# Kernel tuning notes

Hardware: AMD Instinct MI355X
Metric: run time of the kernel (lower is better)

Reference implementation:

```python
import jax, jax.numpy as jnp
import numpy as np

B, T, S = 4, 128, 8192
HID, NH, NKV, HD = 2560, 8, 4, 256
INTER = 10240
WINDOW = 1024
SOFTCAP = 50.0
SCALING = 256 ** -0.5  # query_pre_attn_scalar ** -0.5
EPS = 1e-6
NEG = -2.3819763e38  # large negative for masking (matches Gemma mask value)
ROPE_THETA = 10000.0


def _rmsnorm(x, w):
    xf = x.astype(jnp.float32)
    o = xf * jax.lax.rsqrt(jnp.mean(xf * xf, axis=-1, keepdims=True) + EPS)
    return (o * (1.0 + w.astype(jnp.float32))).astype(x.dtype)


def _rope(x, cos, sin):
    # split-half rotation, matching torch apply_rotary_emb (chunk->complex->mul)
    d2 = x.shape[-1] // 2
    x1, x2 = x[..., :d2], x[..., d2:]
    c = cos[None, :, None, :]  # [1,T,1,D/2]
    s = sin[None, :, None, :]
    return jnp.concatenate([x1 * c - x2 * s, x1 * s + x2 * c], axis=-1)


def setup_inputs() -> dict:
    key = jax.random.key(0)
    ks = jax.random.split(key, 14)
    hidden_states = jax.random.normal(ks[0], (B, T, HID), jnp.float32)
    kv_write_indices = jnp.arange(T, dtype=jnp.int32)
    k_cache = jnp.zeros((B, S, NKV, HD), jnp.float32)
    v_cache = jnp.zeros((B, S, NKV, HD), jnp.float32)
    # rotary tables for positions 0..T-1
    inv = 1.0 / (ROPE_THETA ** (np.arange(0, HD, 2)[: HD // 2].astype(np.float32) / HD))
    fr = np.outer(np.arange(T, dtype=np.float32), inv).astype(np.float32)
    freqs_cos = jnp.asarray(np.cos(fr))
    freqs_sin = jnp.asarray(np.sin(fr))
    # masks: query i sits at absolute position i; cache slots >= T are unwritten
    qpos = jnp.arange(T)[:, None]
    kpos = jnp.arange(S)[None, :]
    causal = kpos <= qpos
    local = causal & ((qpos - kpos) < WINDOW)
    mask = jnp.broadcast_to(jnp.where(causal, 0.0, NEG)[None, None], (B, 1, T, S)).astype(jnp.float32)
    local_mask = jnp.broadcast_to(jnp.where(local, 0.0, NEG)[None, None], (B, 1, T, S)).astype(jnp.float32)
    sc = 0.02
    w_qkv = sc * jax.random.normal(ks[1], ((NH + 2 * NKV) * HD, HID), jnp.float32)
    w_o = sc * jax.random.normal(ks[2], (HID, NH * HD), jnp.float32)
    q_norm_w = 0.1 * jax.random.normal(ks[3], (HD,), jnp.float32)
    k_norm_w = 0.1 * jax.random.normal(ks[4], (HD,), jnp.float32)
    in_ln_w = 0.1 * jax.random.normal(ks[5], (HID,), jnp.float32)
    post_attn_ln_w = 0.1 * jax.random.normal(ks[6], (HID,), jnp.float32)
    pre_ffw_ln_w = 0.1 * jax.random.normal(ks[7], (HID,), jnp.float32)
    post_ffw_ln_w = 0.1 * jax.random.normal(ks[8], (HID,), jnp.float32)
    w_gate = sc * jax.random.normal(ks[9], (INTER, HID), jnp.float32)
    w_up = sc * jax.random.normal(ks[10], (INTER, HID), jnp.float32)
    w_down = sc * jax.random.normal(ks[11], (HID, INTER), jnp.float32)
    return {
        "hidden_states": hidden_states, "freqs_cos": freqs_cos, "freqs_sin": freqs_sin,
        "kv_write_indices": kv_write_indices, "k_cache": k_cache, "v_cache": v_cache,
        "mask": mask, "local_mask": local_mask,
        "w_qkv": w_qkv, "w_o": w_o, "q_norm_w": q_norm_w, "k_norm_w": k_norm_w,
        "in_ln_w": in_ln_w, "post_attn_ln_w": post_attn_ln_w,
        "pre_ffw_ln_w": pre_ffw_ln_w, "post_ffw_ln_w": post_ffw_ln_w,
        "w_gate": w_gate, "w_up": w_up, "w_down": w_down,
    }


def reference(hidden_states, freqs_cos, freqs_sin, kv_write_indices, k_cache, v_cache,
              mask, local_mask, w_qkv, w_o, q_norm_w, k_norm_w, in_ln_w,
              post_attn_ln_w, pre_ffw_ln_w, post_ffw_ln_w, w_gate, w_up, w_down):
    b, t, _ = hidden_states.shape
    residual = hidden_states
    h = _rmsnorm(hidden_states, in_ln_w)
    qkv = h @ w_qkv.T
    q_sz, kv_sz = NH * HD, NKV * HD
    xq = qkv[..., :q_sz].reshape(b, t, NH, HD)
    xk = qkv[..., q_sz:q_sz + kv_sz].reshape(b, t, NKV, HD)
    xv = qkv[..., q_sz + kv_sz:].reshape(b, t, NKV, HD)
    xq = _rmsnorm(xq, q_norm_w)  # QK-norm
    xk = _rmsnorm(xk, k_norm_w)
    xq = _rope(xq, freqs_cos, freqs_sin)
    xk = _rope(xk, freqs_cos, freqs_sin)
    kc = k_cache.at[:, kv_write_indices].set(xk)  # index_copy_ on dim 1
    vc = v_cache.at[:, kv_write_indices].set(xv)
    g = NH // NKV
    q = (xq * SCALING).reshape(b, t, NKV, g, HD)
    # GQA without repeat_interleave: group dim g shares each kv head
    scores = jnp.einsum('btkgd,bskd->bkgts', q, kc)
    scores = SOFTCAP * jnp.tanh(scores / SOFTCAP)  # logit softcapping
    scores = scores + local_mask[:, :, None]  # LOCAL_SLIDING -> use local mask
    probs = jax.nn.softmax(scores.astype(jnp.float32), axis=-1).astype(q.dtype)
    attn = jnp.einsum('bkgts,bskd->btkgd', probs, vc).reshape(b, t, NH * HD)
    attn = attn @ w_o.T
    h = residual + _rmsnorm(attn, post_attn_ln_w)
    residual = h
    x = _rmsnorm(h, pre_ffw_ln_w)
    gate = jax.nn.gelu(x @ w_gate.T, approximate=True)
    mlp = (gate * (x @ w_up.T)) @ w_down.T
    return residual + _rmsnorm(mlp, post_ffw_ln_w)
```

## Files before the change

kernel.cpp:

```cpp
#include <hip/hip_runtime.h>
#include <hip/hip_bf16.h>

#define B_ 4
#define T_ 128
#define HID 2560
#define NH 8
#define NKV 4
#define HD 256
#define INTER 10240
#define MROWS 512
#define EPS 1e-6f

typedef float f32x4 __attribute__((ext_vector_type(4)));
typedef __bf16 bf16x8 __attribute__((ext_vector_type(8)));

__device__ __forceinline__ unsigned short f2bf(float f){
  unsigned int u = __builtin_bit_cast(unsigned int, f);
  u += 0x7fffu + ((u >> 16) & 1u);
  return (unsigned short)(u >> 16);
}
__device__ __forceinline__ float bf2f(unsigned short u){
  unsigned int x = ((unsigned int)u) << 16;
  return __builtin_bit_cast(float, x);
}
__device__ __forceinline__ unsigned int cvtpk(float lo, float hi){
  unsigned int r;
  asm("v_cvt_pk_bf16_f32 %0, %1, %2" : "=v"(r) : "v"(lo), "v"(hi));
  return r;
}
__device__ __forceinline__ void glds16(const void* g, void* l){
  __builtin_amdgcn_global_load_lds(
      (const __attribute__((address_space(1))) void*)g,
      (__attribute__((address_space(3))) void*)l, 16, 0, 0);
}

__device__ __forceinline__ float bsum256(float v, float* buf){
  #pragma unroll
  for (int o = 32; o; o >>= 1) v += __shfl_xor(v, o);
  __syncthreads();
  if ((threadIdx.x & 63) == 0) buf[threadIdx.x >> 6] = v;
  __syncthreads();
  return buf[0] + buf[1] + buf[2] + buf[3];
}


__global__ __launch_bounds__(256) void rms_in(
    const float* __restrict__ x, const float* __restrict__ w,
    unsigned short* __restrict__ out)
{
  __shared__ float buf[4];
  const int r = blockIdx.x, tid = threadIdx.x;
  const float* xp = x + (size_t)r * HID;
  float v[10]; float ss = 0.f;
  #pragma unroll
  for (int j = 0; j < 10; j++){ v[j] = xp[tid + j*256]; ss += v[j]*v[j]; }
  ss = bsum256(ss, buf);
  float s = rsqrtf(ss * (1.f/HID) + EPS);
  #pragma unroll
  for (int j = 0; j < 10; j++){
    int i = tid + j*256;
    out[((size_t)(i >> 5) * MROWS + r) * 32 + (i & 31)] = f2bf(v[j] * s * (1.f + w[i]));
  }
}

__global__ __launch_bounds__(256, 2) void gemm_big(
    const unsigned short* __restrict__ Ap,
    const float* __restrict__ B0,
    const float* __restrict__ B1,
    int n_hi,
    unsigned short* __restrict__ C,
    int N, int K, int klen)
{
  __shared__ char Bs4[4 * 16384];
  const int tid = threadIdx.x;
  const int bid = (blockIdx.x & 7) * ((int)gridDim.x >> 3) + (blockIdx.x >> 3);
  const int bm = (bid & 1) << 8;
  const int bn = (bid >> 1) << 7;
  const int kt0 = (blockIdx.y * klen) >> 5;
  const int nt = klen >> 5;

  const int w = tid >> 6, l = tid & 63;
  const float* Bb = (bn < n_hi) ? B0 : B1;
  const int bnr = (bn < n_hi) ? bn : (bn - n_hi);

  const int grow_l = l >> 3;
  const int gchunk = l & 7;

  const int wm = (w & 1) << 7;
  const int wn = (w >> 1) << 6;
  const int fr = l & 15, kq = l >> 4;

  const unsigned short* ApL = Ap + ((size_t)kt0 * MROWS + bm + wm + fr) * 32 + kq * 8;

  f32x4 acc[8][4];
  #pragma unroll
  for (int i = 0; i < 8; i++)
    #pragma unroll
    for (int j = 0; j < 4; j++)
      #pragma unroll
      for (int e = 0; e < 4; e++) acc[i][j][e] = 0.f;

  uint4 aR[8], aS[8];

#define ISSUE_A(dst, tt) { const unsigned short* ap = ApL + (size_t)(tt) * 16384; \
  dst[0] = *(const uint4*)(ap);        dst[1] = *(const uint4*)(ap + 512); \
  dst[2] = *(const uint4*)(ap + 1024); dst[3] = *(const uint4*)(ap + 1536); \
  dst[4] = *(const uint4*)(ap + 2048); dst[5] = *(const uint4*)(ap + 2560); \
  dst[6] = *(const uint4*)(ap + 3072); dst[7] = *(const uint4*)(ap + 3584); }
#define GLDS_B(tt, slot) { const int ktf = (kt0 + (tt)) << 5; \
  char* dstb = Bs4 + ((slot) << 14) + (w << 12); \
  _Pragma("unroll") for (int g = 0; g < 4; g++){ \
    int row = (w << 5) + (g << 3) + grow_l; \
    const float* src = Bb + (size_t)(bnr + row) * K + ktf + ((gchunk ^ (row & 7)) << 2); \
    glds16(src, dstb + (g << 10)); } }
#define VM(n) asm volatile("s_waitcnt vmcnt(" #n ")" ::: "memory")
#define COMPUTE(slot, aset) { const char* bb = Bs4 + ((slot) << 14); \
  bf16x8 bfv[4]; \
  _Pragma("unroll") for (int ni = 0; ni < 4; ni++){ \
    int row = wn + ni*16 + fr; \
    const char* rbase = bb + (row << 7); \
    int sw = row & 7; \
    f32x4 lo = *(const f32x4*)(rbase + ((( 2*kq   ) ^ sw) << 4)); \
    f32x4 hi = *(const f32x4*)(rbase + ((( 2*kq+1 ) ^ sw) << 4)); \
    union { unsigned int u[4]; bf16x8 v; } pk; \
    pk.u[0] = cvtpk(lo[0], lo[1]); pk.u[1] = cvtpk(lo[2], lo[3]); \
    pk.u[2] = cvtpk(hi[0], hi[1]); pk.u[3] = cvtpk(hi[2], hi[3]); \
    bfv[ni] = pk.v; } \
  __builtin_amdgcn_s_setprio(1); \
  _Pragma("unroll") for (int mi = 0; mi < 8; mi++){ \
    bf16x8 af = __builtin_bit_cast(bf16x8, aset[mi]); \
    _Pragma("unroll") for (int ni = 0; ni < 4; ni++) \
      acc[mi][ni] = __builtin_amdgcn_mfma_f32_16x16x32_bf16(af, bfv[ni], acc[mi][ni], 0, 0, 0); } \
  __builtin_amdgcn_s_setprio(0); }
#define MIN_(a,b) ((a)<(b)?(a):(b))

  ISSUE_A(aR, 0);
  GLDS_B(0, 0); GLDS_B(1, 1); GLDS_B(2, 2);
  ISSUE_A(aS, MIN_(1, nt-1));
  VM(16);
  __builtin_amdgcn_s_barrier();
  GLDS_B(MIN_(3, nt-1), 3);
  COMPUTE(0, aR);
  ISSUE_A(aR, MIN_(2, nt-1));
  VM(24);
  __builtin_amdgcn_s_barrier();
  GLDS_B(MIN_(4, nt-1), 0);
  COMPUTE(1, aS);
  for (int t = 2; t < nt; t += 2) {
    ISSUE_A(aS, MIN_(t+1, nt-1));
    VM(32);
    __builtin_amdgcn_s_barrier();
    GLDS_B(MIN_(t+3, nt-1), (t+3) & 3);
    COMPUTE(t & 3, aR);
    ISSUE_A(aR, MIN_(t+2, nt-1));
    VM(32);
    __builtin_amdgcn_s_barrier();
    GLDS_B(MIN_(t+4, nt-1), t & 3);
    COMPUTE((t+1) & 3, aS);
  }
#undef ISSUE_A
#undef GLDS_B
#undef VM
#undef COMPUTE
#undef MIN_

  unsigned short* Cp = C + (size_t)blockIdx.y * MROWS * N;
  #pragma unroll
  for (int mi = 0; mi < 8; mi++) {
    #pragma unroll
    for (int ni = 0; ni < 4; ni++) {
      int m = bm + wm + mi*16 + kq*4;
      int n = bn + wn + ni*16 + fr;
      #pragma unroll
      for (int i = 0; i < 4; i++)
        Cp[(size_t)(m + i) * N + n] = f2bf(acc[mi][ni][i]);
    }
  }
}

__global__ __launch_bounds__(64) void qkv_post(
    const unsigned short* __restrict__ qkvp,
    const float* __restrict__ fcos, const float* __restrict__ fsin,
    const float* __restrict__ qnw, const float* __restrict__ knw,
    float* __restrict__ qout, float* __restrict__ kT, float* __restrict__ vout)
{
  const int row = blockIdx.x;
  const int hh  = blockIdx.y;
  const int b = row >> 7, t = row & 127;
  const int l = threadIdx.x;
  const size_t MS = (size_t)MROWS * 4096;
  const unsigned short* src = qkvp + (size_t)row * 4096 + hh * 256;
  float x[4];
  #pragma unroll
  for (int j = 0; j < 4; j++){
    int d = l + j*64;
    float v = 0.f;
    #pragma unroll
    for (int s = 0; s < 8; s++) v += bf2f(src[d + s*MS]);
    x[j] = v;
  }
  if (hh >= 12) {
    float* vp = vout + ((size_t)(b*NKV + (hh-12)) * T_ + t) * HD;
    #pragma unroll
    for (int j = 0; j < 4; j++) vp[l + j*64] = x[j];
    return;
  }
  float ss = x[0]*x[0] + x[1]*x[1] + x[2]*x[2] + x[3]*x[3];
  #pragma unroll
  for (int o = 32; o; o >>= 1) ss += __shfl_xor(ss, o);
  float r = rsqrtf(ss * (1.f/HD) + EPS);
  const float* nw = (hh < 8) ? qnw : knw;
  #pragma unroll
  for (int j = 0; j < 4; j++){ int d = l + j*64; x[j] = x[j] * r * (1.f + nw[d]); }
  float c0 = fcos[t*128 + l],      s0 = fsin[t*128 + l];
  float c1 = fcos[t*128 + l + 64], s1 = fsin[t*128 + l + 64];
  float y0 = x[0]*c0 - x[2]*s0;
  float y2 = x[0]*s0 + x[2]*c0;
  float y1 = x[1]*c1 - x[3]*s1;
  float y3 = x[1]*s1 + x[3]*c1;
  if (hh < 8) {
    float* qp = qout + ((size_t)(b*NH + hh) * T_ + t) * HD;
    const float sc = 0.0625f;
    qp[l] = y0*sc; qp[l+64] = y1*sc; qp[l+128] = y2*sc; qp[l+192] = y3*sc;
  } else {
    float* kp = kT + (size_t)(b*NKV + (hh-8)) * HD * T_;
    kp[(size_t)(l)*T_ + t] = y0;  kp[(size_t)(l+64)*T_ + t] = y1;
    kp[(size_t)(l+128)*T_ + t] = y2; kp[(size_t)(l+192)*T_ + t] = y3;
  }
}

__global__ __launch_bounds__(128) void attn_fwd(
    const float* __restrict__ q, const float* __restrict__ kT,
    const float* __restrict__ V, unsigned short* __restrict__ att)
{
  const int id = blockIdx.x;
  const int t = id & 127;
  const int h = (id >> 7) & 7;
  const int b = id >> 10;
  const int kvh = h >> 1;
  const int tid = threadIdx.x;
  __shared__ float qs[256];
  __shared__ float sc[128];
  __shared__ float red[128];
  const float* qp = q + (size_t)id * HD;
  qs[tid] = qp[tid]; qs[tid + 128] = qp[tid + 128];
  __syncthreads();
  const float* kp = kT + (size_t)(b*NKV + kvh) * HD * T_;
  float dot = 0.f;
  const bool valid = (tid <= t);
  if (valid) {
    #pragma unroll 8
    for (int d = 0; d < 256; d++) dot += qs[d] * kp[(size_t)d*T_ + tid];
  }
  float score = valid ? 50.f * tanhf(dot * 0.02f) : -3.0e38f;
  sc[tid] = score; red[tid] = score;
  __syncthreads();
  for (int o = 64; o; o >>= 1){ if (tid < o) red[tid] = fmaxf(red[tid], red[tid+o]); __syncthreads(); }
  float m = red[0];
  __syncthreads();
  float p = valid ? __expf(score - m) : 0.f;
  sc[tid] = p; red[tid] = p;
  __syncthreads();
  for (int o = 64; o; o >>= 1){ if (tid < o) red[tid] += red[tid+o]; __syncthreads(); }
  float inv = 1.f / red[0];
  const float* vp = V + (size_t)(b*NKV + kvh) * T_ * HD;
  float a0 = 0.f, a1 = 0.f;
  for (int s = 0; s <= t; s++){
    float ps = sc[s];
    a0 += ps * vp[(size_t)s*HD + tid];
    a1 += ps * vp[(size_t)s*HD + tid + 128];
  }
  const int row = b*T_ + t;
  const int c0 = h*256 + tid, c1 = c0 + 128;
  att[((size_t)(c0 >> 5) * MROWS + row) * 32 + (c0 & 31)] = f2bf(a0 * inv);
  att[((size_t)(c1 >> 5) * MROWS + row) * 32 + (c1 & 31)] = f2bf(a1 * inv);
}

__global__ __launch_bounds__(256) void post_attn_k(
    const unsigned short* __restrict__ op, const float* __restrict__ hs,
    const float* __restrict__ wpost, const float* __restrict__ wpre,
    float* __restrict__ h2, unsigned short* __restrict__ xout)
{
  __shared__ float buf[4];
  const int r = blockIdx.x, tid = threadIdx.x;
  const size_t MS = (size_t)MROWS * HID;
  float o[10]; float ss = 0.f;
  #pragma unroll
  for (int j = 0; j < 10; j++){
    size_t i = (size_t)r*HID + tid + j*256;
    float v = 0.f;
    #pragma unroll
    for (int s = 0; s < 16; s++) v += bf2f(op[i + s*MS]);
    o[j] = v; ss += v*v;
  }
  ss = bsum256(ss, buf);
  float s = rsqrtf(ss*(1.f/HID) + EPS);
  float h[10]; float s2 = 0.f;
  #pragma unroll
  for (int j = 0; j < 10; j++){
    int i = tid + j*256;
    float hv = hs[(size_t)r*HID + i] + o[j]*s*(1.f + wpost[i]);
    h[j] = hv; h2[(size_t)r*HID + i] = hv; s2 += hv*hv;
  }
  s2 = bsum256(s2, buf);
  float sc2 = rsqrtf(s2*(1.f/HID) + EPS);
  #pragma unroll
  for (int j = 0; j < 10; j++){
    int i = tid + j*256;
    xout[((size_t)(i >> 5) * MROWS + r) * 32 + (i & 31)] = f2bf(h[j]*sc2*(1.f + wpre[i]));
  }
}

__global__ __launch_bounds__(256) void act_fuse(
    const unsigned short* __restrict__ gu,
    unsigned short* __restrict__ act)
{
  const int r = blockIdx.x;
  const int c0 = blockIdx.y * 2560;
  const size_t MS = (size_t)MROWS * 20480;
  const unsigned short* rowp = gu + (size_t)r * 20480;
  for (int c = c0 + threadIdx.x; c < c0 + 2560; c += 256){
    float g = 0.f, u = 0.f;
    #pragma unroll
    for (int s = 0; s < 4; s++){
      g += bf2f(rowp[s*MS + c]);
      u += bf2f(rowp[s*MS + c + INTER]);
    }
    float tt = tanhf(0.7978845608f * (g + 0.044715f * g*g*g));
    float ge = 0.5f * g * (1.f + tt);
    act[((size_t)(c >> 5) * MROWS + r) * 32 + (c & 31)] = f2bf(ge * u);
  }
}

__global__ __launch_bounds__(256) void final_k(
    const unsigned short* __restrict__ dp, const float* __restrict__ h2,
    const float* __restrict__ w, float* __restrict__ out)
{
  __shared__ float buf[4];
  const int r = blockIdx.x, tid = threadIdx.x;
  const size_t MS = (size_t)MROWS * HID;
  float m[10]; float ss = 0.f;
  #pragma unroll
  for (int j = 0; j < 10; j++){
    size_t i = (size_t)r*HID + tid + j*256;
    float v = 0.f;
    #pragma unroll
    for (int s = 0; s < 32; s++) v += bf2f(dp[i + s*MS]);
    m[j] = v; ss += v*v;
  }
  ss = bsum256(ss, buf);
  float s = rsqrtf(ss*(1.f/HID) + EPS);
  #pragma unroll
  for (int j = 0; j < 10; j++){
    int i = tid + j*256;
    out[(size_t)r*HID + i] = h2[(size_t)r*HID + i] + m[j]*s*(1.f + w[i]);
  }
}

extern "C" void kernel_launch(void* const* d_in, const int* in_sizes, int n_in,
                              void* d_out, int out_size, void* d_ws, size_t ws_size,
                              hipStream_t stream)
{
  const float* hs     = (const float*)d_in[0];
  const float* fcos   = (const float*)d_in[1];
  const float* fsin   = (const float*)d_in[2];
  const float* w_qkv  = (const float*)d_in[8];
  const float* w_o    = (const float*)d_in[9];
  const float* qnw    = (const float*)d_in[10];
  const float* knw    = (const float*)d_in[11];
  const float* in_ln  = (const float*)d_in[12];
  const float* w_post = (const float*)d_in[13];
  const float* w_pre  = (const float*)d_in[14];
  const float* w_pffw = (const float*)d_in[15];
  const float* w_gate = (const float*)d_in[16];
  const float* w_up   = (const float*)d_in[17];
  const float* w_down = (const float*)d_in[18];
  float* out = (float*)d_out;

  char* p = (char*)d_ws;
  auto alloc = [&](size_t bytes)->void*{ void* r = p; p += (bytes + 255) & ~(size_t)255; return r; };
  void* P0 = alloc((size_t)4*MROWS*20480*2);
  void* P1 = alloc((size_t)32*MROWS*HID*2);
  unsigned short* h_b   = (unsigned short*)alloc((size_t)MROWS*HID*2);
  float* qbuf           = (float*)alloc((size_t)B_*NH*T_*HD*4);
  float* kT             = (float*)alloc((size_t)B_*NKV*HD*T_*4);
  float* vbuf           = (float*)alloc((size_t)B_*NKV*T_*HD*4);
  unsigned short* att_b = (unsigned short*)alloc((size_t)MROWS*2048*2);
  float* h2             = (float*)alloc((size_t)MROWS*HID*4);
  unsigned short* x_b   = (unsigned short*)alloc((size_t)MROWS*HID*2);
  unsigned short* act_b = (unsigned short*)alloc((size_t)MROWS*INTER*2);

  unsigned short* qkv_p = (unsigned short*)P0;
  unsigned short* gu_p  = (unsigned short*)P0;
  unsigned short* o_p   = (unsigned short*)P1;
  unsigned short* down_p= (unsigned short*)P1;

  rms_in<<<MROWS, 256, 0, stream>>>(hs, in_ln, h_b);
  gemm_big<<<dim3(64, 8), 256, 0, stream>>>(h_b, w_qkv, w_qkv, 1<<30, qkv_p, 4096, 2560, 320);
  qkv_post<<<dim3(MROWS, 16), 64, 0, stream>>>(qkv_p, fcos, fsin, qnw, knw, qbuf, kT, vbuf);
  attn_fwd<<<B_*NH*T_, 128, 0, stream>>>(qbuf, kT, vbuf, att_b);
  gemm_big<<<dim3(40, 16), 256, 0, stream>>>(att_b, w_o, w_o, 1<<30, o_p, 2560, 2048, 128);
  post_attn_k<<<MROWS, 256, 0, stream>>>(o_p, hs, w_post, w_pre, h2, x_b);
  gemm_big<<<dim3(320, 4), 256, 0, stream>>>(x_b, w_gate, w_up, 10240, gu_p, 20480, 2560, 640);
  act_fuse<<<dim3(MROWS, 4), 256, 0, stream>>>(gu_p, act_b);
  gemm_big<<<dim3(40, 32), 256, 0, stream>>>(act_b, w_down, w_down, 1<<30, down_p, 2560, 10240, 320);
  final_k<<<MROWS, 256, 0, stream>>>(down_p, h2, w_pffw, out);
}
```

Baseline: 378.0 us.

## Restructure GEMM to 512-thread blocks covering all rows with LDS-staged A

The GEMM now uses 512-thread blocks, each covering all 512 M rows and a 128-wide N slice. The A operand is double-buffered in LDS via direct global-to-LDS loads instead of being held in registers, and each weight (B) tile is loaded once per block instead of twice. This halves B traffic, which is fp32 and dominates the memory cost, and halves the grid size. In exchange it uses more LDS, runs at one block per CU, and pipelines with a single barrier per k-step, which may expose more latency. Grids not divisible by 8 skip the block-index swizzle.

Measured after the change: 396.5 us. 4.9% more time.

```diff
diff --git a/kernel.cpp b/kernel.cpp
--- a/kernel.cpp
+++ b/kernel.cpp
@@ -63,7 +63,7 @@
   }
 }
 
-__global__ __launch_bounds__(256, 2) void gemm_big(
+__global__ __launch_bounds__(512, 1) void gemm_big(
     const unsigned short* __restrict__ Ap,
     const float* __restrict__ B0,
     const float* __restrict__ B1,
@@ -71,26 +71,23 @@
     unsigned short* __restrict__ C,
     int N, int K, int klen)
 {
-  __shared__ char Bs4[4 * 16384];
+  __shared__ char As[2 * 32768];
+  __shared__ char Bs[4 * 16384];
   const int tid = threadIdx.x;
-  const int bid = (blockIdx.x & 7) * ((int)gridDim.x >> 3) + (blockIdx.x >> 3);
-  const int bm = (bid & 1) << 8;
-  const int bn = (bid >> 1) << 7;
+  const int bid = ((gridDim.x & 7) == 0)
+      ? ((blockIdx.x & 7) * ((int)gridDim.x >> 3) + (blockIdx.x >> 3))
+      : blockIdx.x;
+  const int bn = bid << 7;
   const int kt0 = (blockIdx.y * klen) >> 5;
   const int nt = klen >> 5;
 
   const int w = tid >> 6, l = tid & 63;
+  const int q = w & 3;
+  const int h = w >> 2;
+  const int fr = l & 15, kq = l >> 4;
+
   const float* Bb = (bn < n_hi) ? B0 : B1;
   const int bnr = (bn < n_hi) ? bn : (bn - n_hi);
-
-  const int grow_l = l >> 3;
-  const int gchunk = l & 7;
-
-  const int wm = (w & 1) << 7;
-  const int wn = (w >> 1) << 6;
-  const int fr = l & 15, kq = l >> 4;
-
-  const unsigned short* ApL = Ap + ((size_t)kt0 * MROWS + bm + wm + fr) * 32 + kq * 8;
 
   f32x4 acc[8][4];
   #pragma unroll
@@ -100,65 +97,61 @@
       #pragma unroll
       for (int e = 0; e < 4; e++) acc[i][j][e] = 0.f;
 
-  uint4 aR[8], aS[8];
-
-#define ISSUE_A(dst, tt) { const unsigned short* ap = ApL + (size_t)(tt) * 16384; \
-  dst[0] = *(const uint4*)(ap);        dst[1] = *(const uint4*)(ap + 512); \
-  dst[2] = *(const uint4*)(ap + 1024); dst[3] = *(const uint4*)(ap + 1536); \
-  dst[4] = *(const uint4*)(ap + 2048); dst[5] = *(const uint4*)(ap + 2560); \
-  dst[6] = *(const uint4*)(ap + 3072); dst[7] = *(const uint4*)(ap + 3584); }
-#define GLDS_B(tt, slot) { const int ktf = (kt0 + (tt)) << 5; \
-  char* dstb = Bs4 + ((slot) << 14) + (w << 12); \
-  _Pragma("unroll") for (int g = 0; g < 4; g++){ \
-    int row = (w << 5) + (g << 3) + grow_l; \
-    const float* src = Bb + (size_t)(bnr + row) * K + ktf + ((gchunk ^ (row & 7)) << 2); \
-    glds16(src, dstb + (g << 10)); } }
+#define GLDS_A(tt, slot) { \
+  char* dst = As + ((slot) << 15) + (w << 12); \
+  const size_t kbase = (size_t)(kt0 + (tt)) * MROWS; \
+  _Pragma("unroll") for (int c = 0; c < 4; c++){ \
+    int row = (w << 6) + (c << 4) + (l >> 2); \
+    int j = (l & 3) ^ ((l >> 3) & 3); \
+    const unsigned short* src = Ap + (kbase + row) * 32 + (j << 3); \
+    glds16(src, dst + (c << 10)); } }
+#define GLDS_B(tt, slot) { \
+  char* dst = Bs + ((slot) << 14) + (w << 11); \
+  const int ktf = (kt0 + (tt)) << 5; \
+  _Pragma("unroll") for (int g = 0; g < 2; g++){ \
+    int row = (w << 4) + (g << 3) + (l >> 3); \
+    int j = (l & 7) ^ ((l >> 3) & 7); \
+    const float* src = Bb + (size_t)(bnr + row) * K + ktf + (j << 2); \
+    glds16(src, dst + (g << 10)); } }
 #define VM(n) asm volatile("s_waitcnt vmcnt(" #n ")" ::: "memory")
-#define COMPUTE(slot, aset) { const char* bb = Bs4 + ((slot) << 14); \
-  bf16x8 bfv[4]; \
+#define COMPUTE(sa, sb) { \
+  const char* ab = As + ((sa) << 15); \
+  const char* bb = Bs + ((sb) << 14); \
+  bf16x8 af[8], bfv[4]; \
+  const int ach = (kq ^ ((fr >> 1) & 3)) << 4; \
+  _Pragma("unroll") for (int mi = 0; mi < 8; mi++){ \
+    int row = (q << 7) + mi*16 + fr; \
+    af[mi] = *(const bf16x8*)(ab + (row << 6) + ach); } \
+  const int sw = fr & 7; \
   _Pragma("unroll") for (int ni = 0; ni < 4; ni++){ \
-    int row = wn + ni*16 + fr; \
-    const char* rbase = bb + (row << 7); \
-    int sw = row & 7; \
-    f32x4 lo = *(const f32x4*)(rbase + ((( 2*kq   ) ^ sw) << 4)); \
-    f32x4 hi = *(const f32x4*)(rbase + ((( 2*kq+1 ) ^ sw) << 4)); \
+    int row = (h << 6) + ni*16 + fr; \
+    const char* rb = bb + (row << 7); \
+    f32x4 lo = *(const f32x4*)(rb + ((( 2*kq   ) ^ sw) << 4)); \
+    f32x4 hi = *(const f32x4*)(rb + ((( 2*kq+1 ) ^ sw) << 4)); \
     union { unsigned int u[4]; bf16x8 v; } pk; \
     pk.u[0] = cvtpk(lo[0], lo[1]); pk.u[1] = cvtpk(lo[2], lo[3]); \
     pk.u[2] = cvtpk(hi[0], hi[1]); pk.u[3] = cvtpk(hi[2], hi[3]); \
     bfv[ni] = pk.v; } \
   __builtin_amdgcn_s_setprio(1); \
-  _Pragma("unroll") for (int mi = 0; mi < 8; mi++){ \
-    bf16x8 af = __builtin_bit_cast(bf16x8, aset[mi]); \
+  _Pragma("unroll") for (int mi = 0; mi < 8; mi++) \
     _Pragma("unroll") for (int ni = 0; ni < 4; ni++) \
-      acc[mi][ni] = __builtin_amdgcn_mfma_f32_16x16x32_bf16(af, bfv[ni], acc[mi][ni], 0, 0, 0); } \
+      acc[mi][ni] = __builtin_amdgcn_mfma_f32_16x16x32_bf16(af[mi], bfv[ni], acc[mi][ni], 0, 0, 0); \
   __builtin_amdgcn_s_setprio(0); }
 #define MIN_(a,b) ((a)<(b)?(a):(b))
 
-  ISSUE_A(aR, 0);
+  GLDS_A(0, 0);
   GLDS_B(0, 0); GLDS_B(1, 1); GLDS_B(2, 2);
-  ISSUE_A(aS, MIN_(1, nt-1));
-  VM(16);
+  VM(4);
   __builtin_amdgcn_s_barrier();
-  GLDS_B(MIN_(3, nt-1), 3);
-  COMPUTE(0, aR);
-  ISSUE_A(aR, MIN_(2, nt-1));
-  VM(24);
-  __builtin_amdgcn_s_barrier();
-  GLDS_B(MIN_(4, nt-1), 0);
-  COMPUTE(1, aS);
-  for (int t = 2; t < nt; t += 2) {
-    ISSUE_A(aS, MIN_(t+1, nt-1));
-    VM(32);
+
+  for (int t = 0; t < nt; t++) {
+    GLDS_A(MIN_(t+1, nt-1), (t+1) & 1);
+    GLDS_B(MIN_(t+3, nt-1), (t+3) & 3);
+    COMPUTE(t & 1, t & 3);
+    VM(2);
     __builtin_amdgcn_s_barrier();
-    GLDS_B(MIN_(t+3, nt-1), (t+3) & 3);
-    COMPUTE(t & 3, aR);
-    ISSUE_A(aR, MIN_(t+2, nt-1));
-    VM(32);
-    __builtin_amdgcn_s_barrier();
-    GLDS_B(MIN_(t+4, nt-1), t & 3);
-    COMPUTE((t+1) & 3, aS);
-  }
-#undef ISSUE_A
+  }
+#undef GLDS_A
 #undef GLDS_B
 #undef VM
 #undef COMPUTE
@@ -169,8 +162,8 @@
   for (int mi = 0; mi < 8; mi++) {
     #pragma unroll
     for (int ni = 0; ni < 4; ni++) {
-      int m = bm + wm + mi*16 + kq*4;
-      int n = bn + wn + ni*16 + fr;
+      int m = (q << 7) + mi*16 + kq*4;
+      int n = bn + (h << 6) + ni*16 + fr;
       #pragma unroll
       for (int i = 0; i < 4; i++)
         Cp[(size_t)(m + i) * N + n] = f2bf(acc[mi][ni][i]);
@@ -396,13 +389,13 @@
   unsigned short* down_p= (unsigned short*)P1;
 
   rms_in<<<MROWS, 256, 0, stream>>>(hs, in_ln, h_b);
-  gemm_big<<<dim3(64, 8), 256, 0, stream>>>(h_b, w_qkv, w_qkv, 1<<30, qkv_p, 4096, 2560, 320);
+  gemm_big<<<dim3(32, 8), 512, 0, stream>>>(h_b, w_qkv, w_qkv, 1<<30, qkv_p, 4096, 2560, 320);
   qkv_post<<<dim3(MROWS, 16), 64, 0, stream>>>(qkv_p, fcos, fsin, qnw, knw, qbuf, kT, vbuf);
   attn_fwd<<<B_*NH*T_, 128, 0, stream>>>(qbuf, kT, vbuf, att_b);
-  gemm_big<<<dim3(40, 16), 256, 0, stream>>>(att_b, w_o, w_o, 1<<30, o_p, 2560, 2048, 128);
+  gemm_big<<<dim3(20, 16), 512, 0, stream>>>(att_b, w_o, w_o, 1<<30, o_p, 2560, 2048, 128);
   post_attn_k<<<MROWS, 256, 0, stream>>>(o_p, hs, w_post, w_pre, h2, x_b);
-  gemm_big<<<dim3(320, 4), 256, 0, stream>>>(x_b, w_gate, w_up, 10240, gu_p, 20480, 2560, 640);
+  gemm_big<<<dim3(160, 4), 512, 0, stream>>>(x_b, w_gate, w_up, 10240, gu_p, 20480, 2560, 640);
   act_fuse<<<dim3(MROWS, 4), 256, 0, stream>>>(gu_p, act_b);
-  gemm_big<<<dim3(40, 32), 256, 0, stream>>>(act_b, w_down, w_down, 1<<30, down_p, 2560, 10240, 320);
+  gemm_big<<<dim3(20, 32), 512, 0, stream>>>(act_b, w_down, w_down, 1<<30, down_p, 2560, 10240, 320);
   final_k<<<MROWS, 256, 0, stream>>>(down_p, h2, w_pffw, out);
 }
```
